# Performance work log

Measured on AMD Instinct MI355X. Metric: run time of the kernel, lower is better.

The kernel has to match this reference:

```python
import jax, jax.numpy as jnp
import numpy as np


def conv2d(x, w, b):
    # x: (B,C,H,W), w: (O,I,kh,kw), SAME padding, stride 1
    y = jax.lax.conv_general_dilated(x, w, (1, 1), 'SAME',
                                     dimension_numbers=('NCHW', 'OIHW', 'NCHW'))
    return y + b[None, :, None, None]


def setup_inputs() -> dict:
    key = jax.random.key(0)
    ks = jax.random.split(key, 8)
    B, T, C, H, W = 16, 16, 64, 32, 32
    hd = 64  # hidden_dim == input_dim (required by the module's zero-init of h)

    def winit(k, shape):
        fan_in = shape[1] * shape[2] * shape[3]
        return jax.random.normal(k, shape, jnp.float32) / np.float32(np.sqrt(fan_in))

    return {
        'input_tensor': jax.random.normal(ks[0], (B, T, C, H, W), jnp.float32),
        'time_steps': jnp.arange(T, dtype=jnp.float32),
        'mask': jnp.ones((B, T), jnp.float32),
        # ConvGRUCell params
        'w_gates': winit(ks[1], (2 * hd, C + hd, 3, 3)),
        'b_gates': jnp.zeros((2 * hd,), jnp.float32),
        'w_can': winit(ks[2], (hd, C + hd, 3, 3)),
        'b_can': jnp.zeros((hd,), jnp.float32),
        # ODE func params (tanh(conv3x3(x)))
        'w_ode': winit(ks[3], (hd, hd, 3, 3)),
        'b_ode': jnp.zeros((hd,), jnp.float32),
        # transform_z0: conv1x1 -> ReLU -> conv1x1 (z -> 2z)
        'w_t1': winit(ks[4], (hd, hd, 1, 1)),
        'b_t1': jnp.zeros((hd,), jnp.float32),
        'w_t2': winit(ks[5], (2 * hd, hd, 1, 1)),
        'b_t2': jnp.zeros((2 * hd,), jnp.float32),
    }


def reference(input_tensor, time_steps, mask, w_gates, b_gates, w_can, b_can,
              w_ode, b_ode, w_t1, b_t1, w_t2, b_t2):
    B, T, C, H, W = input_tensor.shape
    hd = w_can.shape[0]

    # run_backwards=True: process i = T-1, T-2, ..., 0
    xs = jnp.flip(input_tensor, axis=1).transpose(1, 0, 2, 3, 4)  # (T,B,C,H,W)
    ms = jnp.flip(mask, axis=1).T                                  # (T,B)
    ts_rev = jnp.flip(time_steps)
    # dt_0 = t_last - (t_last + 0.01) = -0.01 ; dt_k = ts[T-k-1] - ts[T-k]
    dts = jnp.concatenate([jnp.full((1,), -0.01, jnp.float32),
                           ts_rev[1:] - ts_rev[:-1]])               # (T,)

    def step(h, inp):
        x, m, dt = inp
        # Euler ODE step: h_ode = h + ode_func(t, h) * dt
        h_ode = h + jnp.tanh(conv2d(h, w_ode, b_ode)) * dt
        # ConvGRU cell
        comb = jnp.concatenate([x, h_ode], axis=1)
        gates = jax.nn.sigmoid(conv2d(comb, w_gates, b_gates))
        reset, update = gates[:, :hd], gates[:, hd:]
        cand = jnp.tanh(conv2d(jnp.concatenate([x, reset * h_ode], axis=1),
                               w_can, b_can))
        h_new = (1.0 - update) * h_ode + update * cand
        mm = m[:, None, None, None]
        h_next = mm * h_new + (1.0 - mm) * h_ode
        return h_next, None

    h0 = jnp.zeros((B, hd, H, W), input_tensor.dtype)
    last_yi, _ = jax.lax.scan(step, h0, (xs, ms, dts))

    z = jax.nn.relu(conv2d(last_yi, w_t1, b_t1))
    z = conv2d(z, w_t2, b_t2)
    mean_z0 = z[:, :hd]
    std_z0 = jnp.abs(z[:, hd:])
    return mean_z0, std_z0
```

## Files before the change

kernel.cpp:

```cpp
#include <hip/hip_runtime.h>
#include <hip/hip_bf16.h>

#define BB 16
#define TT 16

typedef short short8  __attribute__((ext_vector_type(8)));
typedef short short4v __attribute__((ext_vector_type(4)));
typedef float f32x4   __attribute__((ext_vector_type(4)));

__device__ __forceinline__ ushort f2bf(float f) {
    uint u = __float_as_uint(f);
    u += 0x7FFFu + ((u >> 16) & 1u);
    return (ushort)(u >> 16);
}
__device__ __forceinline__ float bf2f(ushort h) { return __uint_as_float(((uint)h) << 16); }
__device__ __forceinline__ float fast_sigmoid(float x) { return 1.0f / (1.0f + __expf(-x)); }
__device__ __forceinline__ float fast_tanh(float x) {
    float e = __expf(2.0f * x);
    return 1.0f - 2.0f / (e + 1.0f);
}
__device__ __forceinline__ short8 pack8(const float4 a, const float4 b) {
    short8 r;
    r[0]=(short)f2bf(a.x); r[1]=(short)f2bf(a.y); r[2]=(short)f2bf(a.z); r[3]=(short)f2bf(a.w);
    r[4]=(short)f2bf(b.x); r[5]=(short)f2bf(b.y); r[6]=(short)f2bf(b.z); r[7]=(short)f2bf(b.w);
    return r;
}

__global__ __launch_bounds__(256)
void pack_all(const float* __restrict__ wg, const float* __restrict__ wc,
              const float* __restrict__ wo, const float* __restrict__ w1,
              const float* __restrict__ w2,
              ushort* __restrict__ wfX, ushort* __restrict__ wfGh,
              ushort* __restrict__ wfCh, ushort* __restrict__ wfO,
              ushort* __restrict__ wf1, ushort* __restrict__ wf2)
{
    const int gi = blockIdx.x * 256 + threadIdx.x;
    const int fi = gi >> 6, lane = gi & 63;
    if (fi >= 528) return;
    const float* src; ushort* dst;
    int CINfull, ci_base, cb_base, CBn, CBT, NT, lf;
    if (fi < 144)      { lf=fi;     src=wg; dst=wfX;  CINfull=128; ci_base=0;  cb_base=0; CBn=8; CBT=12; NT=9; }
    else if (fi < 216) { lf=fi-144; src=wc; dst=wfX;  CINfull=128; ci_base=0;  cb_base=8; CBn=4; CBT=12; NT=9; }
    else if (fi < 360) { lf=fi-216; src=wg; dst=wfGh; CINfull=128; ci_base=64; cb_base=0; CBn=8; CBT=8;  NT=9; }
    else if (fi < 432) { lf=fi-360; src=wc; dst=wfCh; CINfull=128; ci_base=64; cb_base=0; CBn=4; CBT=4;  NT=9; }
    else if (fi < 504) { lf=fi-432; src=wo; dst=wfO;  CINfull=64;  ci_base=0;  cb_base=0; CBn=4; CBT=4;  NT=9; }
    else if (fi < 512) { lf=fi-504; src=w1; dst=wf1;  CINfull=64;  ci_base=0;  cb_base=0; CBn=4; CBT=4;  NT=1; }
    else               { lf=fi-512; src=w2; dst=wf2;  CINfull=64;  ci_base=0;  cb_base=0; CBn=8; CBT=8;  NT=1; }
    const int KCp = 2;
    const int kc = lf % KCp;
    const int cb = (lf / KCp) % CBn;
    const int tap = lf / (KCp * CBn);
    const int co  = cb * 16 + (lane & 15);
    const int ci0 = ci_base + kc * 32 + (lane >> 4) * 8;
    short8 v;
    #pragma unroll
    for (int e = 0; e < 8; ++e)
        v[e] = (short)f2bf(src[((size_t)co * CINfull + ci0 + e) * NT + tap]);
    const size_t fo = ((size_t)(tap * CBT + cb_base + cb)) * KCp + kc;
    *(short8*)(dst + (fo * 64 + lane) * 8) = v;
}

__global__ __launch_bounds__(256)
void x_transpose(const float* __restrict__ src, ushort* __restrict__ dst) {
    __shared__ float tile[64 * 256];
    const int bt = blockIdx.x, q = blockIdx.y, tid = threadIdx.x;
    const float* s = src + (size_t)bt * 64 * 1024 + q * 256;
    for (int i = tid; i < 64 * 256; i += 256)
        tile[i] = s[(size_t)(i >> 8) * 1024 + (i & 255)];
    __syncthreads();
    const int p = q * 256 + tid;
    ushort* d = dst + ((size_t)bt * 1026 + 1 + p) * 64;
    #pragma unroll
    for (int c8 = 0; c8 < 8; ++c8) {
        short8 v;
        #pragma unroll
        for (int e = 0; e < 8; ++e) v[e] = (short)f2bf(tile[(c8 * 8 + e) * 256 + tid]);
        *(short8*)(d + ((c8 ^ (p & 7)) << 3)) = v;
    }
    if (q == 0 && tid < 8)
        *(short8*)(dst + (size_t)bt * 1026 * 64 + tid * 8) = (short8)0;
    if (q == 3 && tid < 8)
        *(short8*)(dst + ((size_t)bt * 1026 + 1025) * 64 + tid * 8) = (short8)0;
}

__global__ __launch_bounds__(512)
void conv_x192(const ushort* __restrict__ x_cl,
               const ushort* __restrict__ wfX,
               const float* __restrict__ b_gates,
               const float* __restrict__ b_can,
               ushort* __restrict__ axc)
{
    __shared__ ushort sbuf[25600];
    const int rt = blockIdx.x, bt = blockIdx.y;
    const int R  = rt * 4;
    const int tid = threadIdx.x;
    const int w = tid >> 6, lane = tid & 63, lr = lane & 15, lg = lane >> 4;
    const ushort* xbb = x_cl + (size_t)bt * 1026 * 64;

    for (int i = tid; i < 1632; i += 512) {
        const int tr = i / 272, rem = i - tr * 272;
        const int hc = rem >> 3;
        const int y  = R - 1 + tr;
        short8 v = (short8)0;
        if ((unsigned)y < 32u && hc != 0 && hc != 33)
            v = *(const short8*)(xbb + ((size_t)(y * 32 + hc)) * 64 + (rem & 7) * 8);
        *(short8*)(sbuf + (size_t)i * 8) = v;
    }
    __syncthreads();

    const int cb0 = (w & 3) * 3;
    const int pf0 = (w >> 2) * 4;

    f32x4 acc[3][4];
    #pragma unroll
    for (int i = 0; i < 3; ++i)
        #pragma unroll
        for (int j = 0; j < 4; ++j) acc[i][j] = 0;

    #pragma unroll
    for (int tap = 0; tap < 9; ++tap) {
        const int ky = tap / 3, kx = tap - ky * 3;
        #pragma unroll
        for (int kc = 0; kc < 2; ++kc) {
            short8 a[3];
            #pragma unroll
            for (int i = 0; i < 3; ++i)
                a[i] = *(const short8*)(wfX + (size_t)(((tap * 12 + cb0 + i) * 2 + kc) * 512) + lane * 8);
            #pragma unroll
            for (int j = 0; j < 4; ++j) {
                const int px = (pf0 + j) * 16 + lr;
                const int tr = (px >> 5) + ky, hc = (px & 31) + kx;
                short8 bf = *(const short8*)(sbuf + (tr * 34 + hc) * 64 + (((kc * 4 + lg) ^ ((hc + 7) & 7)) << 3));
                #pragma unroll
                for (int i = 0; i < 3; ++i)
                    acc[i][j] = __builtin_amdgcn_mfma_f32_16x16x32_bf16(a[i], bf, acc[i][j], 0, 0, 0);
            }
        }
    }
    __syncthreads();

    #pragma unroll
    for (int i = 0; i < 3; ++i) {
        const int co0 = (cb0 + i) * 16 + lg * 4;
        const float* bsrc = (co0 < 128) ? (b_gates + co0) : (b_can + co0 - 128);
        const f32x4 b4 = *(const f32x4*)bsrc;
        #pragma unroll
        for (int j = 0; j < 4; ++j) {
            const int px = (pf0 + j) * 16 + lr;
            short4v s;
            #pragma unroll
            for (int r = 0; r < 4; ++r)
                s[r] = (short)f2bf(acc[i][j][r] + b4[r]);
            *(short4v*)(sbuf + px * 200 + co0) = s;
        }
    }
    __syncthreads();

    ushort* dst = axc + (((size_t)bt * 1024) + R * 32) * 192;
    for (int i = tid; i < 3072; i += 512) {
        const int px = i / 24, c = i - px * 24;
        *(short8*)(dst + (size_t)px * 192 + c * 8) = *(const short8*)(sbuf + px * 200 + c * 8);
    }
}

__global__ __launch_bounds__(512, 1)
void fused_step(const ushort* __restrict__ axc,
                const float* __restrict__ h_in,
                const ushort* __restrict__ h_inb,
                float* __restrict__ h_out,
                ushort* __restrict__ h_outb,
                const ushort* __restrict__ wfO,
                const ushort* __restrict__ wfGh,
                const ushort* __restrict__ wfCh,
                const float* __restrict__ b_ode,
                const float* __restrict__ tsteps,
                const float* __restrict__ mask,
                int t)
{
    extern __shared__ ushort smem[];
    float*  smemf = (float*)smem;
    ushort* hbuf  = smem;
    ushort* obuf  = smem + 17408;
    ushort* rhbuf = smem;
    float*  ubuf  = smemf + 4352;
    float*  hode  = smemf + 15232;

    const int rt = blockIdx.x, b = blockIdx.y;
    const int R  = rt * 2;
    const int tid = threadIdx.x;
    const int w = tid >> 6, lane = tid & 63, lr = lane & 15, lg = lane >> 4;
    const int bti = b * TT + (TT - 1 - t);

    const ushort* hbb = h_inb + (size_t)b * 1026 * 64;
    const float*  hb  = h_in  + (size_t)b * 65536;
    const ushort* axb = axc + (size_t)bti * 1024 * 192;

    short4v gxr[2][4], cxr[2];
    {
        const int cq = w & 3, ph = w >> 2;
        #pragma unroll
        for (int i = 0; i < 2; ++i) {
            const int cog0 = (2 * cq + i) * 16 + lg * 4;
            #pragma unroll
            for (int j = 0; j < 4; ++j) {
                const int f = 4 * ph + j;
                const int y = R - 1 + (f >> 1);
                const int c = (f & 1) * 16 + lr;
                short4v g = (short4v)0;
                if ((unsigned)y < 32u)
                    g = *(const short4v*)(axb + ((size_t)(y * 32 + c)) * 192 + cog0);
                gxr[i][j] = g;
            }
        }
        const int cf = w & 3, ph2 = w >> 2;
        const int co0 = cf * 16 + lg * 4;
        #pragma unroll
        for (int j = 0; j < 2; ++j) {
            const int c = j * 16 + lr;
            const int pix = (R + (ph2 & 1)) * 32 + c;
            cxr[j] = *(const short4v*)(axb + (size_t)pix * 192 + 128 + co0);
        }
    }

    for (int i = tid; i < 2176; i += 512) {
        const int tr = i / 272, rem = i - tr * 272;
        const int hc = rem >> 3;
        const int y  = R - 3 + tr;
        short8 v = (short8)0;
        if ((unsigned)y < 32u && hc != 0 && hc != 33)
            v = *(const short8*)(hbb + ((size_t)(y * 32 + hc)) * 64 + (rem & 7) * 8);
        *(short8*)(hbuf + (size_t)i * 8) = v;
    }
    for (int i = tid; i < 1632; i += 512) {
        const int tr = i / 272, rem = i - tr * 272;
        const int hc = rem >> 3;
        const int y  = R - 2 + tr;
        if (hc == 0 || hc == 33 || (unsigned)y >= 32u)
            *(short8*)(obuf + (size_t)i * 8) = (short8)0;
    }
    __syncthreads();

    {
        const int cb0 = (w & 1) * 2;
        const int pxg = w >> 1;
        f32x4 accA[2][3];
        #pragma unroll
        for (int i = 0; i < 2; ++i)
            #pragma unroll
            for (int j = 0; j < 3; ++j) accA[i][j] = 0;

        #pragma unroll
        for (int tap = 0; tap < 9; ++tap) {
            const int ky = tap / 3, kx = tap - ky * 3;
            #pragma unroll
            for (int kc = 0; kc < 2; ++kc) {
                short8 a0 = *(const short8*)(wfO + (size_t)(((tap * 4 + cb0 + 0) * 2 + kc) * 512) + lane * 8);
                short8 a1 = *(const short8*)(wfO + (size_t)(((tap * 4 + cb0 + 1) * 2 + kc) * 512) + lane * 8);
                #pragma unroll
                for (int j = 0; j < 3; ++j) {
                    const int p  = (3 * pxg + j) * 16 + lr;
                    const int tr = (p >> 5) + ky, hc = (p & 31) + kx;
                    short8 bf = *(const short8*)(hbuf + (tr * 34 + hc) * 64 + ((((kc << 2) + lg) ^ ((hc + 7) & 7)) << 3));
                    accA[0][j] = __builtin_amdgcn_mfma_f32_16x16x32_bf16(a0, bf, accA[0][j], 0, 0, 0);
                    accA[1][j] = __builtin_amdgcn_mfma_f32_16x16x32_bf16(a1, bf, accA[1][j], 0, 0, 0);
                }
            }
        }
        const float dt = (t == 0) ? -0.01f : (tsteps[TT - 1 - t] - tsteps[TT - t]);
        #pragma unroll
        for (int i = 0; i < 2; ++i) {
            #pragma unroll
            for (int j = 0; j < 3; ++j) {
                const int co0 = (cb0 + i) * 16 + lg * 4;
                const int p = (3 * pxg + j) * 16 + lr;
                const int orow = p >> 5, c = p & 31;
                const int y = R - 2 + orow;
                if ((unsigned)y < 32u) {
                    const f32x4 h4 = *(const f32x4*)(hb + ((size_t)(y * 32 + c)) * 64 + co0);
                    const f32x4 b4 = *(const f32x4*)(b_ode + co0);
                    f32x4 ho;
                    #pragma unroll
                    for (int r = 0; r < 4; ++r)
                        ho[r] = h4[r] + fast_tanh(accA[i][j][r] + b4[r]) * dt;
                    short4v s;
                    #pragma unroll
                    for (int r = 0; r < 4; ++r) s[r] = (short)f2bf(ho[r]);
                    *(short4v*)(obuf + (orow * 34 + c + 1) * 64 + (((co0 >> 3) ^ (c & 7)) << 3) + (co0 & 7)) = s;
                    if ((unsigned)(y - R) < 2u)
                        *(f32x4*)(hode + ((y - R) * 32 + c) * 64 + (((co0 >> 2) ^ (c & 15)) << 2)) = ho;
                }
            }
        }
    }
    __syncthreads();

    for (int i = tid; i < 1088; i += 512) {
        const int tr = i / 272, rem = i - tr * 272;
        const int hc = rem >> 3;
        const int y  = R - 1 + tr;
        if (hc == 0 || hc == 33 || (unsigned)y >= 32u)
            *(short8*)(rhbuf + (size_t)i * 8) = (short8)0;
    }

    {
        const int cq = w & 3, ph = w >> 2;
        f32x4 accB[2][4];
        #pragma unroll
        for (int i = 0; i < 2; ++i)
            #pragma unroll
            for (int j = 0; j < 4; ++j) {
                f32x4 g;
                #pragma unroll
                for (int r = 0; r < 4; ++r) g[r] = bf2f((ushort)gxr[i][j][r]);
                accB[i][j] = g;
            }

        #pragma unroll
        for (int tap = 0; tap < 9; ++tap) {
            const int ky = tap / 3, kx = tap - ky * 3;
            #pragma unroll
            for (int kc = 0; kc < 2; ++kc) {
                short8 a0 = *(const short8*)(wfGh + (size_t)(((tap * 8 + 2 * cq + 0) * 2 + kc) * 512) + lane * 8);
                short8 a1 = *(const short8*)(wfGh + (size_t)(((tap * 8 + 2 * cq + 1) * 2 + kc) * 512) + lane * 8);
                #pragma unroll
                for (int j = 0; j < 4; ++j) {
                    const int f  = 4 * ph + j;
                    const int tr = (f >> 1) + ky;
                    const int hc = (f & 1) * 16 + lr + kx;
                    short8 bf = *(const short8*)(obuf + (tr * 34 + hc) * 64 + ((((kc << 2) + lg) ^ ((hc + 7) & 7)) << 3));
                    accB[0][j] = __builtin_amdgcn_mfma_f32_16x16x32_bf16(a0, bf, accB[0][j], 0, 0, 0);
                    accB[1][j] = __builtin_amdgcn_mfma_f32_16x16x32_bf16(a1, bf, accB[1][j], 0, 0, 0);
                }
            }
        }
        #pragma unroll
        for (int i = 0; i < 2; ++i) {
            const int cog = (2 * cq + i) * 16 + lg * 4;
            #pragma unroll
            for (int j = 0; j < 4; ++j) {
                const int f = 4 * ph + j;
                const int y = R - 1 + (f >> 1);
                const int c = (f & 1) * 16 + lr;
                if (cq < 2) {
                    if ((unsigned)y < 32u) {
                        const int tro = (f >> 1) + 1;
                        const int key = (((cog >> 3) ^ (c & 7)) << 3) + (cog & 7);
                        short4v ho4 = *(const short4v*)(obuf + (tro * 34 + c + 1) * 64 + key);
                        short4v s;
                        #pragma unroll
                        for (int r = 0; r < 4; ++r)
                            s[r] = (short)f2bf(fast_sigmoid(accB[i][j][r]) * bf2f((ushort)ho4[r]));
                        *(short4v*)(rhbuf + ((f >> 1) * 34 + c + 1) * 64 + key) = s;
                    }
                } else if ((unsigned)(y - R) < 2u) {
                    const int cu = cog - 64;
                    f32x4 u;
                    #pragma unroll
                    for (int r = 0; r < 4; ++r)
                        u[r] = fast_sigmoid(accB[i][j][r]);
                    *(f32x4*)(ubuf + ((y - R) * 32 + c) * 64 + (((cu >> 2) ^ (c & 15)) << 2)) = u;
                }
            }
        }
    }
    __syncthreads();

    {
        const int cf = w & 3, ph2 = w >> 2;
        const int co0 = cf * 16 + lg * 4;
        f32x4 accC[2];
        #pragma unroll
        for (int j = 0; j < 2; ++j) {
            f32x4 g;
            #pragma unroll
            for (int r = 0; r < 4; ++r) g[r] = bf2f((ushort)cxr[j][r]);
            accC[j] = g;
        }

        #pragma unroll
        for (int tap = 0; tap < 9; ++tap) {
            const int ky = tap / 3, kx = tap - ky * 3;
            #pragma unroll
            for (int kc = 0; kc < 2; ++kc) {
                short8 a = *(const short8*)(wfCh + (size_t)(((tap * 4 + cf) * 2 + kc) * 512) + lane * 8);
                #pragma unroll
                for (int j = 0; j < 2; ++j) {
                    const int tr = ph2 + ky;
                    const int hc = j * 16 + lr + kx;
                    short8 bf = *(const short8*)(rhbuf + (tr * 34 + hc) * 64 + ((((kc << 2) + lg) ^ ((hc + 7) & 7)) << 3));
                    accC[j] = __builtin_amdgcn_mfma_f32_16x16x32_bf16(a, bf, accC[j], 0, 0, 0);
                }
            }
        }
        const float m = mask[b * TT + (TT - 1 - t)];
        const int y = R + ph2;
        #pragma unroll
        for (int j = 0; j < 2; ++j) {
            const int c = j * 16 + lr;
            const int pi = ph2 * 32 + c;
            const int sw = ((co0 >> 2) ^ (c & 15)) << 2;
            const f32x4 ho = *(const f32x4*)(hode + pi * 64 + sw);
            const f32x4 u  = *(const f32x4*)(ubuf + pi * 64 + sw);
            f32x4 o;
            short4v s;
            #pragma unroll
            for (int r = 0; r < 4; ++r) {
                const float cand = fast_tanh(accC[j][r]);
                o[r] = ho[r] + m * u[r] * (cand - ho[r]);
                s[r] = (short)f2bf(o[r]);
            }
            const int pix = y * 32 + c;
            *(f32x4*)(h_out + (size_t)b * 65536 + (size_t)pix * 64 + co0) = o;
            *(short4v*)(h_outb + ((size_t)b * 1026 + 1 + pix) * 64
                        + (((co0 >> 3) ^ (c & 7)) << 3) + (co0 & 7)) = s;
        }
    }
}

__global__ __launch_bounds__(256)
void head_mfma(const float* __restrict__ h,
               const ushort* __restrict__ w1f, const float* __restrict__ b1,
               const ushort* __restrict__ w2f, const float* __restrict__ b2,
               float* __restrict__ outp)
{
    __shared__ ushort hlds[64 * 64];
    __shared__ ushort zlds[64 * 64];
    const int blk = blockIdx.x, b = blk >> 4, pixb = (blk & 15) * 64;
    const int tid = threadIdx.x, wv = tid >> 6, lane = tid & 63, lr = lane & 15, lg = lane >> 4;
    const float* hb = h + ((size_t)b * 1024 + pixb) * 64;

    for (int idx = tid; idx < 64 * 8; idx += 256) {
        const int c = idx & 7, px = idx >> 3;
        const float4* p = (const float4*)(hb + (size_t)px * 64 + c * 8);
        *(short8*)(hlds + px * 64 + ((c ^ (px & 7)) << 3)) = pack8(p[0], p[1]);
    }
    __syncthreads();

    f32x4 acc1[4]; acc1[0]=0; acc1[1]=0; acc1[2]=0; acc1[3]=0;
    #pragma unroll
    for (int kc = 0; kc < 2; ++kc) {
        short8 a = *(const short8*)(w1f + (((size_t)wv * 2 + kc) * 64 + lane) * 8);
        #pragma unroll
        for (int p = 0; p < 4; ++p) {
            const int hp = p * 16 + lr;
            short8 bf = *(const short8*)(hlds + hp * 64 + (((kc * 4 + lg) ^ (hp & 7)) << 3));
            acc1[p] = __builtin_amdgcn_mfma_f32_16x16x32_bf16(a, bf, acc1[p], 0, 0, 0);
        }
    }
    {
        const int co0 = wv * 16 + lg * 4;
        const f32x4 b4 = *(const f32x4*)(b1 + co0);
        #pragma unroll
        for (int p = 0; p < 4; ++p) {
            const int px = p * 16 + lr;
            short4v s;
            #pragma unroll
            for (int r = 0; r < 4; ++r)
                s[r] = (short)f2bf(fmaxf(acc1[p][r] + b4[r], 0.0f));
            *(short4v*)(zlds + px * 64 + (((co0 >> 3) ^ (px & 7)) << 3) + (co0 & 7)) = s;
        }
    }
    __syncthreads();

    f32x4 acc2[2][4];
    #pragma unroll
    for (int gi = 0; gi < 2; ++gi)
        #pragma unroll
        for (int p = 0; p < 4; ++p) acc2[gi][p] = 0;
    #pragma unroll
    for (int kc = 0; kc < 2; ++kc) {
        short8 a0 = *(const short8*)(w2f + ((((size_t)wv * 2 + 0) * 2 + kc) * 64 + lane) * 8);
        short8 a1 = *(const short8*)(w2f + ((((size_t)wv * 2 + 1) * 2 + kc) * 64 + lane) * 8);
        #pragma unroll
        for (int p = 0; p < 4; ++p) {
            const int hp = p * 16 + lr;
            short8 bf = *(const short8*)(zlds + hp * 64 + (((kc * 4 + lg) ^ (hp & 7)) << 3));
            acc2[0][p] = __builtin_amdgcn_mfma_f32_16x16x32_bf16(a0, bf, acc2[0][p], 0, 0, 0);
            acc2[1][p] = __builtin_amdgcn_mfma_f32_16x16x32_bf16(a1, bf, acc2[1][p], 0, 0, 0);
        }
    }
    #pragma unroll
    for (int gi = 0; gi < 2; ++gi) {
        const int co0 = wv * 32 + gi * 16 + lg * 4;
        const f32x4 b4 = *(const f32x4*)(b2 + co0);
        #pragma unroll
        for (int p = 0; p < 4; ++p) {
            const int px = pixb + p * 16 + lr;
            #pragma unroll
            for (int r = 0; r < 4; ++r) {
                const int co = co0 + r;
                const float v = acc2[gi][p][r] + b4[r];
                if (co < 64)
                    outp[((size_t)b * 64 + co) * 1024 + px] = v;
                else
                    outp[(size_t)BB * 64 * 1024 + ((size_t)b * 64 + (co - 64)) * 1024 + px] = fabsf(v);
            }
        }
    }
}

extern "C" void kernel_launch(void* const* d_in, const int* in_sizes, int n_in,
                              void* d_out, int out_size, void* d_ws, size_t ws_size,
                              hipStream_t stream)
{
    const float* xall    = (const float*)d_in[0];
    const float* tsteps  = (const float*)d_in[1];
    const float* mask    = (const float*)d_in[2];
    const float* w_gates = (const float*)d_in[3];
    const float* b_gates = (const float*)d_in[4];
    const float* w_can   = (const float*)d_in[5];
    const float* b_can   = (const float*)d_in[6];
    const float* w_ode   = (const float*)d_in[7];
    const float* b_ode   = (const float*)d_in[8];
    const float* w_t1    = (const float*)d_in[9];
    const float* b_t1    = (const float*)d_in[10];
    const float* w_t2    = (const float*)d_in[11];
    const float* b_t2    = (const float*)d_in[12];
    float* out = (float*)d_out;

    float*  h0   = (float*)d_ws;
    float*  h1   = h0 + (size_t)BB * 65536;
    ushort* h0b  = (ushort*)(h1 + (size_t)BB * 65536);
    ushort* h1b  = h0b + (size_t)BB * 1026 * 64;
    ushort* axc  = h1b + (size_t)BB * 1026 * 64;
    ushort* x_cl = axc + (size_t)256 * 1024 * 192;
    ushort* wfX  = x_cl + (size_t)BB * TT * 1026 * 64;
    ushort* wfGh = wfX  + (size_t)216 * 512;
    ushort* wfCh = wfGh + (size_t)144 * 512;
    ushort* wfO  = wfCh + (size_t)72 * 512;
    ushort* wf1  = wfO  + (size_t)72 * 512;
    ushort* wf2  = wf1  + (size_t)8 * 512;

    hipMemsetAsync(h0, 0, (size_t)BB * 65536 * sizeof(float), stream);
    hipMemsetAsync(h0b, 0, (size_t)BB * 1026 * 64 * 2 * sizeof(ushort), stream);

    x_transpose<<<dim3(256, 4), 256, 0, stream>>>(xall, x_cl);
    pack_all<<<dim3(132), 256, 0, stream>>>(w_gates, w_can, w_ode, w_t1, w_t2,
                                            wfX, wfGh, wfCh, wfO, wf1, wf2);
    conv_x192<<<dim3(8, 256), 512, 0, stream>>>(x_cl, wfX, b_gates, b_can, axc);

    hipFuncSetAttribute(reinterpret_cast<const void*>(fused_step),
                        hipFuncAttributeMaxDynamicSharedMemorySize, 77312);

    for (int t = 0; t < TT; ++t) {
        const float*  hin   = (t & 1) ? h1  : h0;
        float*        hout  = (t & 1) ? h0  : h1;
        const ushort* hinb  = (t & 1) ? h1b : h0b;
        ushort*       houtb = (t & 1) ? h0b : h1b;
        fused_step<<<dim3(16, BB), 512, 77312, stream>>>(axc, hin, hinb, hout, houtb,
                                                         wfO, wfGh, wfCh,
                                                         b_ode, tsteps, mask, t);
    }
    head_mfma<<<dim3(256), 256, 0, stream>>>(h0, wf1, b_t1, wf2, b_t2, out);
}
```

Measured before the change: 450.6 us.

## Fuse input transpose into x-convolution and read halo h from LDS

Removes the separate x_transpose kernel and its bf16 channel-last intermediate buffer. conv_x now loads fp32 input rows straight into shared memory and converts and swizzles them there before the MFMA loop. In fused_step, halo rows of h are taken from the bf16 copy already in LDS rather than reloaded as fp32 from global memory, which adds some bf16 rounding to the ODE update on halo pixels. The head kernel's pack8 helper is inlined. The larger dynamic shared memory in conv_x may lower occupancy.

```diff
diff --git a/kernel.cpp b/kernel.cpp
--- a/kernel.cpp
+++ b/kernel.cpp
@@ -18,12 +18,6 @@
 __device__ __forceinline__ float fast_tanh(float x) {
     float e = __expf(2.0f * x);
     return 1.0f - 2.0f / (e + 1.0f);
-}
-__device__ __forceinline__ short8 pack8(const float4 a, const float4 b) {
-    short8 r;
-    r[0]=(short)f2bf(a.x); r[1]=(short)f2bf(a.y); r[2]=(short)f2bf(a.z); r[3]=(short)f2bf(a.w);
-    r[4]=(short)f2bf(b.x); r[5]=(short)f2bf(b.y); r[6]=(short)f2bf(b.z); r[7]=(short)f2bf(b.w);
-    return r;
 }
 
 __global__ __launch_bounds__(256)
@@ -60,51 +54,45 @@
     *(short8*)(dst + (fo * 64 + lane) * 8) = v;
 }
 
-__global__ __launch_bounds__(256)
-void x_transpose(const float* __restrict__ src, ushort* __restrict__ dst) {
-    __shared__ float tile[64 * 256];
-    const int bt = blockIdx.x, q = blockIdx.y, tid = threadIdx.x;
-    const float* s = src + (size_t)bt * 64 * 1024 + q * 256;
-    for (int i = tid; i < 64 * 256; i += 256)
-        tile[i] = s[(size_t)(i >> 8) * 1024 + (i & 255)];
-    __syncthreads();
-    const int p = q * 256 + tid;
-    ushort* d = dst + ((size_t)bt * 1026 + 1 + p) * 64;
-    #pragma unroll
-    for (int c8 = 0; c8 < 8; ++c8) {
-        short8 v;
-        #pragma unroll
-        for (int e = 0; e < 8; ++e) v[e] = (short)f2bf(tile[(c8 * 8 + e) * 256 + tid]);
-        *(short8*)(d + ((c8 ^ (p & 7)) << 3)) = v;
-    }
-    if (q == 0 && tid < 8)
-        *(short8*)(dst + (size_t)bt * 1026 * 64 + tid * 8) = (short8)0;
-    if (q == 3 && tid < 8)
-        *(short8*)(dst + ((size_t)bt * 1026 + 1025) * 64 + tid * 8) = (short8)0;
-}
-
 __global__ __launch_bounds__(512)
-void conv_x192(const ushort* __restrict__ x_cl,
-               const ushort* __restrict__ wfX,
-               const float* __restrict__ b_gates,
-               const float* __restrict__ b_can,
-               ushort* __restrict__ axc)
+void conv_x(const float* __restrict__ xall,
+            const ushort* __restrict__ wfX,
+            const float* __restrict__ b_gates,
+            const float* __restrict__ b_can,
+            ushort* __restrict__ axc)
 {
-    __shared__ ushort sbuf[25600];
+    extern __shared__ ushort smem[];
+    ushort* xb   = smem;
+    float*  fraw = (float*)(smem + 13056);
+    ushort* outb = smem + 13056;
+
     const int rt = blockIdx.x, bt = blockIdx.y;
     const int R  = rt * 4;
     const int tid = threadIdx.x;
     const int w = tid >> 6, lane = tid & 63, lr = lane & 15, lg = lane >> 4;
-    const ushort* xbb = x_cl + (size_t)bt * 1026 * 64;
+    const float* xs = xall + (size_t)bt * 65536;
+
+    for (int i = tid; i < 3072; i += 512) {
+        const int ch = i / 48, rem = i - ch * 48;
+        const int tr = rem >> 3, q = rem & 7;
+        const int y = R - 1 + tr;
+        if ((unsigned)y < 32u)
+            *(float4*)(fraw + ch * 203 + tr * 32 + q * 4) =
+                *(const float4*)(xs + (size_t)ch * 1024 + y * 32 + q * 4);
+    }
+    __syncthreads();
 
     for (int i = tid; i < 1632; i += 512) {
         const int tr = i / 272, rem = i - tr * 272;
-        const int hc = rem >> 3;
-        const int y  = R - 1 + tr;
+        const int hc = rem >> 3, c8 = rem & 7;
+        const int y = R - 1 + tr, x = hc - 1;
         short8 v = (short8)0;
-        if ((unsigned)y < 32u && hc != 0 && hc != 33)
-            v = *(const short8*)(xbb + ((size_t)(y * 32 + hc)) * 64 + (rem & 7) * 8);
-        *(short8*)(sbuf + (size_t)i * 8) = v;
+        if ((unsigned)y < 32u && (unsigned)x < 32u) {
+            #pragma unroll
+            for (int e = 0; e < 8; ++e)
+                v[e] = (short)f2bf(fraw[(c8 * 8 + e) * 203 + tr * 32 + x]);
+        }
+        *(short8*)(xb + (tr * 34 + hc) * 64 + ((c8 ^ ((hc + 7) & 7)) << 3)) = v;
     }
     __syncthreads();
 
@@ -130,7 +118,7 @@
             for (int j = 0; j < 4; ++j) {
                 const int px = (pf0 + j) * 16 + lr;
                 const int tr = (px >> 5) + ky, hc = (px & 31) + kx;
-                short8 bf = *(const short8*)(sbuf + (tr * 34 + hc) * 64 + (((kc * 4 + lg) ^ ((hc + 7) & 7)) << 3));
+                short8 bf = *(const short8*)(xb + (tr * 34 + hc) * 64 + (((kc * 4 + lg) ^ ((hc + 7) & 7)) << 3));
                 #pragma unroll
                 for (int i = 0; i < 3; ++i)
                     acc[i][j] = __builtin_amdgcn_mfma_f32_16x16x32_bf16(a[i], bf, acc[i][j], 0, 0, 0);
@@ -151,7 +139,7 @@
             #pragma unroll
             for (int r = 0; r < 4; ++r)
                 s[r] = (short)f2bf(acc[i][j][r] + b4[r]);
-            *(short4v*)(sbuf + px * 200 + co0) = s;
+            *(short4v*)(outb + px * 200 + co0) = s;
         }
     }
     __syncthreads();
@@ -159,7 +147,7 @@
     ushort* dst = axc + (((size_t)bt * 1024) + R * 32) * 192;
     for (int i = tid; i < 3072; i += 512) {
         const int px = i / 24, c = i - px * 24;
-        *(short8*)(dst + (size_t)px * 192 + c * 8) = *(const short8*)(sbuf + px * 200 + c * 8);
+        *(short8*)(dst + (size_t)px * 192 + c * 8) = *(const short8*)(outb + px * 200 + c * 8);
     }
 }
 
@@ -276,7 +264,15 @@
                 const int orow = p >> 5, c = p & 31;
                 const int y = R - 2 + orow;
                 if ((unsigned)y < 32u) {
-                    const f32x4 h4 = *(const f32x4*)(hb + ((size_t)(y * 32 + c)) * 64 + co0);
+                    const int key = (((co0 >> 3) ^ (c & 7)) << 3) + (co0 & 7);
+                    f32x4 h4;
+                    if ((unsigned)(y - R) < 2u) {
+                        h4 = *(const f32x4*)(hb + ((size_t)(y * 32 + c)) * 64 + co0);
+                    } else {
+                        short4v hv = *(const short4v*)(hbuf + ((orow + 1) * 34 + c + 1) * 64 + key);
+                        #pragma unroll
+                        for (int r = 0; r < 4; ++r) h4[r] = bf2f((ushort)hv[r]);
+                    }
                     const f32x4 b4 = *(const f32x4*)(b_ode + co0);
                     f32x4 ho;
                     #pragma unroll
@@ -285,7 +281,7 @@
                     short4v s;
                     #pragma unroll
                     for (int r = 0; r < 4; ++r) s[r] = (short)f2bf(ho[r]);
-                    *(short4v*)(obuf + (orow * 34 + c + 1) * 64 + (((co0 >> 3) ^ (c & 7)) << 3) + (co0 & 7)) = s;
+                    *(short4v*)(obuf + (orow * 34 + c + 1) * 64 + key) = s;
                     if ((unsigned)(y - R) < 2u)
                         *(f32x4*)(hode + ((y - R) * 32 + c) * 64 + (((co0 >> 2) ^ (c & 15)) << 2)) = ho;
                 }
@@ -432,7 +428,10 @@
     for (int idx = tid; idx < 64 * 8; idx += 256) {
         const int c = idx & 7, px = idx >> 3;
         const float4* p = (const float4*)(hb + (size_t)px * 64 + c * 8);
-        *(short8*)(hlds + px * 64 + ((c ^ (px & 7)) << 3)) = pack8(p[0], p[1]);
+        short8 v;
+        #pragma unroll
+        for (int e = 0; e < 4; ++e) { v[e] = (short)f2bf(((const float*)p)[e]); v[e+4] = (short)f2bf(((const float*)p)[e+4]); }
+        *(short8*)(hlds + px * 64 + ((c ^ (px & 7)) << 3)) = v;
     }
     __syncthreads();
 
@@ -523,8 +522,7 @@
     ushort* h0b  = (ushort*)(h1 + (size_t)BB * 65536);
     ushort* h1b  = h0b + (size_t)BB * 1026 * 64;
     ushort* axc  = h1b + (size_t)BB * 1026 * 64;
-    ushort* x_cl = axc + (size_t)256 * 1024 * 192;
-    ushort* wfX  = x_cl + (size_t)BB * TT * 1026 * 64;
+    ushort* wfX  = axc + (size_t)256 * 1024 * 192;
     ushort* wfGh = wfX  + (size_t)216 * 512;
     ushort* wfCh = wfGh + (size_t)144 * 512;
     ushort* wfO  = wfCh + (size_t)72 * 512;
@@ -534,10 +532,12 @@
     hipMemsetAsync(h0, 0, (size_t)BB * 65536 * sizeof(float), stream);
     hipMemsetAsync(h0b, 0, (size_t)BB * 1026 * 64 * 2 * sizeof(ushort), stream);
 
-    x_transpose<<<dim3(256, 4), 256, 0, stream>>>(xall, x_cl);
     pack_all<<<dim3(132), 256, 0, stream>>>(w_gates, w_can, w_ode, w_t1, w_t2,
                                             wfX, wfGh, wfCh, wfO, wf1, wf2);
-    conv_x192<<<dim3(8, 256), 512, 0, stream>>>(x_cl, wfX, b_gates, b_can, axc);
+
+    hipFuncSetAttribute(reinterpret_cast<const void*>(conv_x),
+                        hipFuncAttributeMaxDynamicSharedMemorySize, 78080);
+    conv_x<<<dim3(8, 256), 512, 78080, stream>>>(xall, wfX, b_gates, b_can, axc);
 
     hipFuncSetAttribute(reinterpret_cast<const void*>(fused_step),
                         hipFuncAttributeMaxDynamicSharedMemorySize, 77312);
```

Result: faster. 417.3 us (-7.4%).
